# Optimization experiments

Hardware: AMD Instinct MI355X
Metric: run time of the kernel (lower is better)

Reference implementation:

```python
import jax, jax.numpy as jnp
import numpy as np

B, T, D, H = 4, 2048, 1024, 16
DH = D // H


def setup_inputs() -> dict:
    key = jax.random.key(0)
    ks = jax.random.split(key, 5)
    x = jax.random.normal(ks[0], (B, T, D), dtype=jnp.float32)
    W_qkv = jax.random.normal(ks[1], (D, 3 * D), dtype=jnp.float32) * 0.02
    b_qkv = jax.random.normal(ks[2], (3 * D,), dtype=jnp.float32) * 0.02
    W_o = jax.random.normal(ks[3], (D, D), dtype=jnp.float32) * 0.02
    b_o = jax.random.normal(ks[4], (D,), dtype=jnp.float32) * 0.02
    return {"x": x, "W_qkv": W_qkv, "b_qkv": b_qkv, "W_o": W_o, "b_o": b_o}


def reference(x, W_qkv, b_qkv, W_o, b_o):
    b, t, d = x.shape
    qkv = x @ W_qkv + b_qkv                      # [b, t, 3*d]
    # 'b t (k h dh) -> k b h t dh'
    qkv = qkv.reshape(b, t, 3, H, DH).transpose(2, 0, 3, 1, 4)
    q, k, v = qkv[0], qkv[1], qkv[2]             # each [b, h, t, dh]
    scores = jnp.einsum('bhqd,bhkd->bhqk', q, k) / jnp.sqrt(jnp.float32(DH))
    causal_mask = jnp.triu(jnp.ones((t, t), dtype=bool), k=1)  # True above diag
    scores = jnp.where(causal_mask, -jnp.inf, scores)
    attn = jax.nn.softmax(scores, axis=-1)       # [b, h, t, t]
    o = jnp.einsum('bhqk,bhkd->bqhd', attn, v).reshape(b, t, d)
    return o @ W_o + b_o
```

## Files before the change

kernel.cpp:

```cpp
#include <hip/hip_runtime.h>
#include <hip/hip_bf16.h>

typedef __attribute__((ext_vector_type(8))) short bh8;
typedef __attribute__((ext_vector_type(4))) float f32x4;

#define GBL(p) (const __attribute__((address_space(1))) void*)(p)
#define LDSP(p) (__attribute__((address_space(3))) void*)(p)

__device__ __forceinline__ ushort f2bf(float f){
  union { float f; unsigned u; } v; v.f = f;
  unsigned u = v.u;
  return (ushort)((u + 0x7fffu + ((u >> 16) & 1u)) >> 16);
}

__global__ __launch_bounds__(256) void cast_x_kernel(const float4* __restrict__ in,
                                                     ushort* __restrict__ out){
  int i = blockIdx.x * 256 + threadIdx.x;
  float4 v = in[i];
  ushort4 o;
  o.x = f2bf(v.x); o.y = f2bf(v.y); o.z = f2bf(v.z); o.w = f2bf(v.w);
  *(ushort4*)&out[(size_t)i * 4] = o;
}

__global__ __launch_bounds__(256) void transpose_cast_kernel(const float* __restrict__ in,
                                                             ushort* __restrict__ out,
                                                             int R, int C){
  __shared__ float tile[32][33];
  int bx = blockIdx.x * 32;
  int by = blockIdx.y * 32;
  int tx = threadIdx.x, ty = threadIdx.y;
  #pragma unroll
  for (int i = 0; i < 32; i += 8)
    tile[ty + i][tx] = in[(size_t)(by + ty + i) * C + bx + tx];
  __syncthreads();
  #pragma unroll
  for (int i = 0; i < 32; i += 8)
    out[(size_t)(bx + ty + i) * R + by + tx] = f2bf(tile[tx][ty + i]);
}

__global__ __launch_bounds__(256, 4) void gemm_qkv_kernel(
    const ushort* __restrict__ A,
    const ushort* __restrict__ Bt,
    const float* __restrict__ bias,
    ushort* __restrict__ Qd, ushort* __restrict__ Kd, ushort* __restrict__ Vt)
{
  constexpr int K = 1024;
  __shared__ ushort sA[2][4096];
  __shared__ ushort sB[2][4096];
  const int tid = threadIdx.x;
  const int lane = tid & 63, wave = tid >> 6;
  const int quad = lane >> 4, l16 = lane & 15;
  const int wm = (wave >> 1) * 64, wn = (wave & 1) * 64;
  const size_t aBase = (size_t)blockIdx.x * 128 * K;
  const size_t bBase = (size_t)blockIdx.y * 128 * K;

  const int u0 = tid, u1 = 256 + tid;
  const int r0 = u0 >> 2, c0 = (u0 & 3) ^ ((r0 ^ (r0 >> 2)) & 3);
  const int r1 = u1 >> 2, c1 = (u1 & 3) ^ ((r1 ^ (r1 >> 2)) & 3);
  const ushort* a0 = A + aBase + (size_t)r0 * K + c0 * 8;
  const ushort* a1 = A + aBase + (size_t)r1 * K + c1 * 8;
  const ushort* b0 = Bt + bBase + (size_t)r0 * K + c0 * 8;
  const ushort* b1 = Bt + bBase + (size_t)r1 * K + c1 * 8;

  int aoff[4], boff[4];
  #pragma unroll
  for (int i = 0; i < 4; i++){
    int ra = wm + i * 16 + l16;
    aoff[i] = (ra * 4 + (quad ^ ((ra ^ (ra >> 2)) & 3))) * 8;
    int rb = wn + i * 16 + l16;
    boff[i] = (rb * 4 + (quad ^ ((rb ^ (rb >> 2)) & 3))) * 8;
  }

  f32x4 acc[4][4] = {};
  __builtin_amdgcn_global_load_lds(GBL(a0), LDSP(&sA[0][u0 * 8]), 16, 0, 0);
  __builtin_amdgcn_global_load_lds(GBL(a1), LDSP(&sA[0][u1 * 8]), 16, 0, 0);
  __builtin_amdgcn_global_load_lds(GBL(b0), LDSP(&sB[0][u0 * 8]), 16, 0, 0);
  __builtin_amdgcn_global_load_lds(GBL(b1), LDSP(&sB[0][u1 * 8]), 16, 0, 0);
  asm volatile("s_waitcnt vmcnt(0)" ::: "memory");
  __builtin_amdgcn_s_barrier();

  #pragma unroll 2
  for (int t = 0; t < 32; t++){
    const int cur = t & 1;
    if (t < 31){
      const int nb = cur ^ 1, ko = (t + 1) * 32;
      __builtin_amdgcn_global_load_lds(GBL(a0 + ko), LDSP(&sA[nb][u0 * 8]), 16, 0, 0);
      __builtin_amdgcn_global_load_lds(GBL(a1 + ko), LDSP(&sA[nb][u1 * 8]), 16, 0, 0);
      __builtin_amdgcn_global_load_lds(GBL(b0 + ko), LDSP(&sB[nb][u0 * 8]), 16, 0, 0);
      __builtin_amdgcn_global_load_lds(GBL(b1 + ko), LDSP(&sB[nb][u1 * 8]), 16, 0, 0);
    }
    bh8 af[4], bf[4];
    #pragma unroll
    for (int i = 0; i < 4; i++) af[i] = *(const bh8*)&sA[cur][aoff[i]];
    #pragma unroll
    for (int j = 0; j < 4; j++) bf[j] = *(const bh8*)&sB[cur][boff[j]];
    __builtin_amdgcn_s_setprio(1);
    #pragma unroll
    for (int i = 0; i < 4; i++)
      #pragma unroll
      for (int j = 0; j < 4; j++)
        acc[i][j] = __builtin_amdgcn_mfma_f32_16x16x32_bf16(af[i], bf[j], acc[i][j], 0, 0, 0);
    __builtin_amdgcn_s_setprio(0);
    asm volatile("s_waitcnt vmcnt(0)" ::: "memory");
    __builtin_amdgcn_s_barrier();
  }

  const int whichBlk = (blockIdx.y * 128) >> 10;
  #pragma unroll
  for (int i = 0; i < 4; i++){
    int mg = blockIdx.x * 128 + wm + i * 16 + quad * 4;
    int bb = mg >> 11, t0 = mg & 2047;
    #pragma unroll
    for (int j = 0; j < 4; j++){
      int ng = blockIdx.y * 128 + wn + j * 16 + l16;
      float bv = bias[ng];
      int h = (ng >> 6) & 15;
      int dh = ng & 63;
      if (whichBlk == 2){
        ushort4 o;
        o.x = f2bf(acc[i][j][0] + bv);
        o.y = f2bf(acc[i][j][1] + bv);
        o.z = f2bf(acc[i][j][2] + bv);
        o.w = f2bf(acc[i][j][3] + bv);
        *(ushort4*)&Vt[((size_t)((bb * 16 + h) * 64 + dh)) * 2048 + t0] = o;
      } else {
        ushort* dst = (whichBlk == 0) ? Qd : Kd;
        float sc = (whichBlk == 0) ? 0.18033688f : 1.0f;
        #pragma unroll
        for (int r = 0; r < 4; r++)
          dst[((size_t)((bb * 16 + h) * 2048 + t0 + r) << 6) + dh] = f2bf((acc[i][j][r] + bv) * sc);
      }
    }
  }
}

__global__ __launch_bounds__(256, 4) void flash_attn_kernel(
    const ushort* __restrict__ Qd, const ushort* __restrict__ Kd,
    const ushort* __restrict__ Vt, ushort* __restrict__ Od)
{
  __shared__ ushort sK[2][4096];
  __shared__ ushort sV[2][4096];
  __shared__ ushort sP[4][1024];
  const int tid = threadIdx.x;
  const int lane = tid & 63, wave = tid >> 6;
  const int quad = lane >> 4, l16 = lane & 15;
  const int bh = blockIdx.x, pairI = blockIdx.y;
  const size_t base = (size_t)bh * (2048 * 64);
  const float SINIT = -7.2134752f;

  const int p0 = tid, p1 = 256 + tid;
  const int r0 = p0 >> 3, c0 = (p0 & 7) ^ (r0 & 7);
  const int r1 = p1 >> 3, c1 = (p1 & 7) ^ (r1 & 7);
  const ushort* kp0 = Kd + base + r0 * 64 + c0 * 8;
  const ushort* kp1 = Kd + base + r1 * 64 + c1 * 8;
  const ushort* vp0 = Vt + base + (size_t)r0 * 2048 + c0 * 8;
  const ushort* vp1 = Vt + base + (size_t)r1 * 2048 + c1 * 8;

  const int b = bh >> 4, h = bh & 15;

  int poff[4];
  #pragma unroll
  for (int j = 0; j < 4; j++){
    int cu = 2 * j + (quad >> 1);
    poff[j] = (l16 * 8 + (cu ^ (l16 & 7))) * 8 + (quad & 1) * 4;
  }

  #pragma unroll 1
  for (int phase = 0; phase < 2; phase++){
    const int qt = phase ? pairI : (31 - pairI);
    const ushort* qrow = Qd + base + (size_t)(qt * 64 + wave * 16 + l16) * 64 + quad * 8;
    bh8 qf0 = *(const bh8*)qrow;
    bh8 qf1 = *(const bh8*)(qrow + 32);

    f32x4 Oacc[4] = {};
    float lsum = 0.f;

    __syncthreads();
    __builtin_amdgcn_global_load_lds(GBL(kp0), LDSP(&sK[0][p0 * 8]), 16, 0, 0);
    __builtin_amdgcn_global_load_lds(GBL(kp1), LDSP(&sK[0][p1 * 8]), 16, 0, 0);
    __builtin_amdgcn_global_load_lds(GBL(vp0), LDSP(&sV[0][p0 * 8]), 16, 0, 0);
    __builtin_amdgcn_global_load_lds(GBL(vp1), LDSP(&sV[0][p1 * 8]), 16, 0, 0);

    #pragma unroll 1
    for (int kt = 0; kt <= qt; kt++){
      const int buf = kt & 1;
      __syncthreads();
      if (kt < qt){
        const int nb = buf ^ 1;
        __builtin_amdgcn_global_load_lds(GBL(kp0 + (kt + 1) * 4096), LDSP(&sK[nb][p0 * 8]), 16, 0, 0);
        __builtin_amdgcn_global_load_lds(GBL(kp1 + (kt + 1) * 4096), LDSP(&sK[nb][p1 * 8]), 16, 0, 0);
        __builtin_amdgcn_global_load_lds(GBL(vp0 + (kt + 1) * 64),   LDSP(&sV[nb][p0 * 8]), 16, 0, 0);
        __builtin_amdgcn_global_load_lds(GBL(vp1 + (kt + 1) * 64),   LDSP(&sV[nb][p1 * 8]), 16, 0, 0);
      }
      f32x4 S[4];
      #pragma unroll
      for (int j = 0; j < 4; j++) S[j] = (f32x4){SINIT, SINIT, SINIT, SINIT};
      __builtin_amdgcn_s_setprio(1);
      #pragma unroll
      for (int ks = 0; ks < 2; ks++){
        bh8 aq = ks ? qf1 : qf0;
        #pragma unroll
        for (int j = 0; j < 4; j++){
          int row = j * 16 + l16;
          int u = row * 8 + ((ks * 4 + quad) ^ (row & 7));
          bh8 bk = *(const bh8*)&sK[buf][u * 8];
          S[j] = __builtin_amdgcn_mfma_f32_16x16x32_bf16(bk, aq, S[j], 0, 0, 0);
        }
      }
      __builtin_amdgcn_s_setprio(0);
      if (kt == qt){
        const int relq = wave * 16 + l16;
        #pragma unroll
        for (int j = 0; j < 4; j++)
          #pragma unroll
          for (int r = 0; r < 4; r++){
            int relt = j * 16 + quad * 4 + r;
            if (relt > relq) S[j][r] = -1e30f;
          }
      }
      #pragma unroll
      for (int j = 0; j < 4; j++){
        float pv[4];
        #pragma unroll
        for (int r = 0; r < 4; r++){
          pv[r] = exp2f(S[j][r]);
          lsum += pv[r];
        }
        __hip_bfloat162 pk0 = __float22bfloat162_rn({pv[0], pv[1]});
        __hip_bfloat162 pk1 = __float22bfloat162_rn({pv[2], pv[3]});
        ushort2 w0 = *(ushort2*)&pk0, w1 = *(ushort2*)&pk1;
        ushort4 o4; o4.x = w0.x; o4.y = w0.y; o4.z = w1.x; o4.w = w1.y;
        *(ushort4*)&sP[wave][poff[j]] = o4;
      }
      __builtin_amdgcn_s_setprio(1);
      #pragma unroll
      for (int ks = 0; ks < 2; ks++){
        int up = l16 * 8 + ((ks * 4 + quad) ^ (l16 & 7));
        bh8 ap = *(const bh8*)&sP[wave][up * 8];
        #pragma unroll
        for (int j = 0; j < 4; j++){
          int row = j * 16 + l16;
          int u = row * 8 + ((ks * 4 + quad) ^ (row & 7));
          bh8 bv = *(const bh8*)&sV[buf][u * 8];
          Oacc[j] = __builtin_amdgcn_mfma_f32_16x16x32_bf16(ap, bv, Oacc[j], 0, 0, 0);
        }
      }
      __builtin_amdgcn_s_setprio(0);
    }
    float s = lsum;
    s += __shfl_xor(s, 16, 64);
    s += __shfl_xor(s, 32, 64);
    float lr[4];
    #pragma unroll
    for (int r = 0; r < 4; r++)
      lr[r] = 1.0f / __shfl(s, quad * 4 + r, 64);
    #pragma unroll
    for (int j = 0; j < 4; j++)
      #pragma unroll
      for (int r = 0; r < 4; r++){
        int qg = qt * 64 + wave * 16 + quad * 4 + r;
        int dh = j * 16 + l16;
        Od[(size_t)(b * 2048 + qg) * 1024 + h * 64 + dh] = f2bf(Oacc[j][r] * lr[r]);
      }
  }
}

__global__ __launch_bounds__(256, 4) void gemm_out_kernel(
    const ushort* __restrict__ A,
    const ushort* __restrict__ Bt,
    const float* __restrict__ bias,
    float* __restrict__ out)
{
  constexpr int K = 1024;
  __shared__ ushort sA[2][4096];
  __shared__ ushort sB[2][4096];
  const int tid = threadIdx.x;
  const int lane = tid & 63, wave = tid >> 6;
  const int quad = lane >> 4, l16 = lane & 15;
  const int wm = (wave >> 1) * 64, wn = (wave & 1) * 64;
  const size_t aBase = (size_t)blockIdx.x * 128 * K;
  const size_t bBase = (size_t)blockIdx.y * 128 * K;

  const int u0 = tid, u1 = 256 + tid;
  const int r0 = u0 >> 2, c0 = (u0 & 3) ^ ((r0 ^ (r0 >> 2)) & 3);
  const int r1 = u1 >> 2, c1 = (u1 & 3) ^ ((r1 ^ (r1 >> 2)) & 3);
  const ushort* a0 = A + aBase + (size_t)r0 * K + c0 * 8;
  const ushort* a1 = A + aBase + (size_t)r1 * K + c1 * 8;
  const ushort* b0 = Bt + bBase + (size_t)r0 * K + c0 * 8;
  const ushort* b1 = Bt + bBase + (size_t)r1 * K + c1 * 8;

  int aoff[4], boff[4];
  #pragma unroll
  for (int i = 0; i < 4; i++){
    int ra = wm + i * 16 + l16;
    aoff[i] = (ra * 4 + (quad ^ ((ra ^ (ra >> 2)) & 3))) * 8;
    int rb = wn + i * 16 + l16;
    boff[i] = (rb * 4 + (quad ^ ((rb ^ (rb >> 2)) & 3))) * 8;
  }

  f32x4 acc[4][4] = {};
  __builtin_amdgcn_global_load_lds(GBL(a0), LDSP(&sA[0][u0 * 8]), 16, 0, 0);
  __builtin_amdgcn_global_load_lds(GBL(a1), LDSP(&sA[0][u1 * 8]), 16, 0, 0);
  __builtin_amdgcn_global_load_lds(GBL(b0), LDSP(&sB[0][u0 * 8]), 16, 0, 0);
  __builtin_amdgcn_global_load_lds(GBL(b1), LDSP(&sB[0][u1 * 8]), 16, 0, 0);
  asm volatile("s_waitcnt vmcnt(0)" ::: "memory");
  __builtin_amdgcn_s_barrier();

  #pragma unroll 2
  for (int t = 0; t < 32; t++){
    const int cur = t & 1;
    if (t < 31){
      const int nb = cur ^ 1, ko = (t + 1) * 32;
      __builtin_amdgcn_global_load_lds(GBL(a0 + ko), LDSP(&sA[nb][u0 * 8]), 16, 0, 0);
      __builtin_amdgcn_global_load_lds(GBL(a1 + ko), LDSP(&sA[nb][u1 * 8]), 16, 0, 0);
      __builtin_amdgcn_global_load_lds(GBL(b0 + ko), LDSP(&sB[nb][u0 * 8]), 16, 0, 0);
      __builtin_amdgcn_global_load_lds(GBL(b1 + ko), LDSP(&sB[nb][u1 * 8]), 16, 0, 0);
    }
    bh8 af[4], bf[4];
    #pragma unroll
    for (int i = 0; i < 4; i++) af[i] = *(const bh8*)&sA[cur][aoff[i]];
    #pragma unroll
    for (int j = 0; j < 4; j++) bf[j] = *(const bh8*)&sB[cur][boff[j]];
    __builtin_amdgcn_s_setprio(1);
    #pragma unroll
    for (int i = 0; i < 4; i++)
      #pragma unroll
      for (int j = 0; j < 4; j++)
        acc[i][j] = __builtin_amdgcn_mfma_f32_16x16x32_bf16(af[i], bf[j], acc[i][j], 0, 0, 0);
    __builtin_amdgcn_s_setprio(0);
    asm volatile("s_waitcnt vmcnt(0)" ::: "memory");
    __builtin_amdgcn_s_barrier();
  }

  #pragma unroll
  for (int i = 0; i < 4; i++){
    int gm = blockIdx.x * 128 + wm + i * 16 + quad * 4;
    #pragma unroll
    for (int j = 0; j < 4; j++){
      int ng = blockIdx.y * 128 + wn + j * 16 + l16;
      float bv = bias[ng];
      #pragma unroll
      for (int r = 0; r < 4; r++)
        out[(size_t)(gm + r) * 1024 + ng] = acc[i][j][r] + bv;
    }
  }
}

extern "C" void kernel_launch(void* const* d_in, const int* in_sizes, int n_in,
                              void* d_out, int out_size, void* d_ws, size_t ws_size,
                              hipStream_t stream) {
  const float* x    = (const float*)d_in[0];
  const float* Wqkv = (const float*)d_in[1];
  const float* bqkv = (const float*)d_in[2];
  const float* Wo   = (const float*)d_in[3];
  const float* bo   = (const float*)d_in[4];
  float* out = (float*)d_out;

  char* p = (char*)d_ws;
  ushort* xb  = (ushort*)p;
  ushort* WqT = (ushort*)(p + 16777216);
  ushort* WoT = (ushort*)(p + 16777216 + 6291456);
  ushort* Qd  = (ushort*)(p + 25165824);
  ushort* Kd  = (ushort*)(p + 25165824 + 16777216);
  ushort* Vt  = (ushort*)(p + 25165824 + 33554432);
  ushort* Od  = xb;

  cast_x_kernel<<<8192, 256, 0, stream>>>((const float4*)x, xb);
  transpose_cast_kernel<<<dim3(96, 32), dim3(32, 8), 0, stream>>>(Wqkv, WqT, 1024, 3072);
  transpose_cast_kernel<<<dim3(32, 32), dim3(32, 8), 0, stream>>>(Wo, WoT, 1024, 1024);
  gemm_qkv_kernel<<<dim3(64, 24), 256, 0, stream>>>(xb, WqT, bqkv, Qd, Kd, Vt);
  flash_attn_kernel<<<dim3(64, 16), 256, 0, stream>>>(Qd, Kd, Vt, Od);
  gemm_out_kernel<<<dim3(64, 8), 256, 0, stream>>>(Od, WoT, bo, out);
}
```

Baseline: 252.5 us.

## Remap GEMM block IDs for XCD locality and re-swizzle attention P buffer

```diff
diff --git a/kernel.cpp b/kernel.cpp
--- a/kernel.cpp
+++ b/kernel.cpp
@@ -51,8 +51,11 @@
   const int lane = tid & 63, wave = tid >> 6;
   const int quad = lane >> 4, l16 = lane & 15;
   const int wm = (wave >> 1) * 64, wn = (wave & 1) * 64;
-  const size_t aBase = (size_t)blockIdx.x * 128 * K;
-  const size_t bBase = (size_t)blockIdx.y * 128 * K;
+  const int orig = blockIdx.y * 64 + blockIdx.x;
+  const int id = (orig & 7) * 192 + (orig >> 3);
+  const int bx = id & 63, by = id >> 6;
+  const size_t aBase = (size_t)bx * 128 * K;
+  const size_t bBase = (size_t)by * 128 * K;
 
   const int u0 = tid, u1 = 256 + tid;
   const int r0 = u0 >> 2, c0 = (u0 & 3) ^ ((r0 ^ (r0 >> 2)) & 3);
@@ -105,14 +108,14 @@
     __builtin_amdgcn_s_barrier();
   }
 
-  const int whichBlk = (blockIdx.y * 128) >> 10;
+  const int whichBlk = (by * 128) >> 10;
   #pragma unroll
   for (int i = 0; i < 4; i++){
-    int mg = blockIdx.x * 128 + wm + i * 16 + quad * 4;
+    int mg = bx * 128 + wm + i * 16 + quad * 4;
     int bb = mg >> 11, t0 = mg & 2047;
     #pragma unroll
     for (int j = 0; j < 4; j++){
-      int ng = blockIdx.y * 128 + wn + j * 16 + l16;
+      int ng = by * 128 + wn + j * 16 + l16;
       float bv = bias[ng];
       int h = (ng >> 6) & 15;
       int dh = ng & 63;
@@ -158,11 +161,16 @@
 
   const int b = bh >> 4, h = bh & 15;
 
-  int poff[4];
-  #pragma unroll
-  for (int j = 0; j < 4; j++){
-    int cu = 2 * j + (quad >> 1);
-    poff[j] = (l16 * 8 + (cu ^ (l16 & 7))) * 8 + (quad & 1) * 4;
+  int woff[4];
+  #pragma unroll
+  for (int j = 0; j < 4; j++)
+    woff[j] = (l16 * 16 + ((4 * j + quad) ^ l16)) * 4;
+  int roff[2][2];
+  #pragma unroll
+  for (int ks = 0; ks < 2; ks++){
+    int hu = (ks * 4 + quad) * 2;
+    roff[ks][0] = (l16 * 16 + (hu ^ l16)) * 4;
+    roff[ks][1] = (l16 * 16 + ((hu + 1) ^ l16)) * 4;
   }
 
   #pragma unroll 1
@@ -173,7 +181,7 @@
     bh8 qf1 = *(const bh8*)(qrow + 32);
 
     f32x4 Oacc[4] = {};
-    float lsum = 0.f;
+    float lp[4] = {0.f, 0.f, 0.f, 0.f};
 
     __syncthreads();
     __builtin_amdgcn_global_load_lds(GBL(kp0), LDSP(&sK[0][p0 * 8]), 16, 0, 0);
@@ -224,30 +232,31 @@
         #pragma unroll
         for (int r = 0; r < 4; r++){
           pv[r] = exp2f(S[j][r]);
-          lsum += pv[r];
+          lp[r] += pv[r];
         }
         __hip_bfloat162 pk0 = __float22bfloat162_rn({pv[0], pv[1]});
         __hip_bfloat162 pk1 = __float22bfloat162_rn({pv[2], pv[3]});
         ushort2 w0 = *(ushort2*)&pk0, w1 = *(ushort2*)&pk1;
         ushort4 o4; o4.x = w0.x; o4.y = w0.y; o4.z = w1.x; o4.w = w1.y;
-        *(ushort4*)&sP[wave][poff[j]] = o4;
+        *(ushort4*)&sP[wave][woff[j]] = o4;
       }
       __builtin_amdgcn_s_setprio(1);
       #pragma unroll
       for (int ks = 0; ks < 2; ks++){
-        int up = l16 * 8 + ((ks * 4 + quad) ^ (l16 & 7));
-        bh8 ap = *(const bh8*)&sP[wave][up * 8];
+        union { ushort4 hh[2]; bh8 v; } pu;
+        pu.hh[0] = *(const ushort4*)&sP[wave][roff[ks][0]];
+        pu.hh[1] = *(const ushort4*)&sP[wave][roff[ks][1]];
         #pragma unroll
         for (int j = 0; j < 4; j++){
           int row = j * 16 + l16;
           int u = row * 8 + ((ks * 4 + quad) ^ (row & 7));
           bh8 bv = *(const bh8*)&sV[buf][u * 8];
-          Oacc[j] = __builtin_amdgcn_mfma_f32_16x16x32_bf16(ap, bv, Oacc[j], 0, 0, 0);
+          Oacc[j] = __builtin_amdgcn_mfma_f32_16x16x32_bf16(pu.v, bv, Oacc[j], 0, 0, 0);
         }
       }
       __builtin_amdgcn_s_setprio(0);
     }
-    float s = lsum;
+    float s = (lp[0] + lp[1]) + (lp[2] + lp[3]);
     s += __shfl_xor(s, 16, 64);
     s += __shfl_xor(s, 32, 64);
     float lr[4];
@@ -278,8 +287,11 @@
   const int lane = tid & 63, wave = tid >> 6;
   const int quad = lane >> 4, l16 = lane & 15;
   const int wm = (wave >> 1) * 64, wn = (wave & 1) * 64;
-  const size_t aBase = (size_t)blockIdx.x * 128 * K;
-  const size_t bBase = (size_t)blockIdx.y * 128 * K;
+  const int orig = blockIdx.y * 64 + blockIdx.x;
+  const int id = (orig & 7) * 64 + (orig >> 3);
+  const int bx = id & 63, by = id >> 6;
+  const size_t aBase = (size_t)bx * 128 * K;
+  const size_t bBase = (size_t)by * 128 * K;
 
   const int u0 = tid, u1 = 256 + tid;
   const int r0 = u0 >> 2, c0 = (u0 & 3) ^ ((r0 ^ (r0 >> 2)) & 3);
@@ -334,10 +346,10 @@
 
   #pragma unroll
   for (int i = 0; i < 4; i++){
-    int gm = blockIdx.x * 128 + wm + i * 16 + quad * 4;
+    int gm = bx * 128 + wm + i * 16 + quad * 4;
     #pragma unroll
     for (int j = 0; j < 4; j++){
-      int ng = blockIdx.y * 128 + wn + j * 16 + l16;
+      int ng = by * 128 + wn + j * 16 + l16;
       float bv = bias[ng];
       #pragma unroll
       for (int r = 0; r < 4; r++)
```

Result: slower. 277.3 us (+9.8%).
